# Kernel tuning notes

Measured on AMD Instinct MI355X. Metric: run time of the kernel, lower is better.

## Reference

```python
import jax, jax.numpy as jnp
import numpy as np

ALPHA = 0.2          # LeakyReLU negative slope
NEG_INF = -9e15      # mask value used by the original pygat implementation


def gat_layer(x, adj, W, a_src, a_dst, concat):
    """Dense multi-head GAT layer (pygat-style GraphAttentionLayer).

    x: [N, F_in], adj: [N, N] bool, W: [K, F_in, H], a_src/a_dst: [K, H].
    Returns [N, K*H] (concat=True, with ELU) or [N, H] (concat=False, mean heads).
    """
    h = jnp.einsum('nf,kfh->knh', x, W)                      # [K, N, H]
    f_src = jnp.einsum('knh,kh->kn', h, a_src)               # [K, N]
    f_dst = jnp.einsum('knh,kh->kn', h, a_dst)               # [K, N]
    e = jax.nn.leaky_relu(f_src[:, :, None] + f_dst[:, None, :], ALPHA)  # [K, N, N]
    e = jnp.where(adj[None, :, :], e, NEG_INF)
    att = jax.nn.softmax(e, axis=-1)                         # masked softmax over neighbors
    out = jnp.einsum('knm,kmh->knh', att, h)                 # [K, N, H]
    if concat:
        K, N, H = out.shape
        return jax.nn.elu(jnp.transpose(out, (1, 0, 2)).reshape(N, K * H))
    return out.mean(axis=0)                                  # [N, H]


def setup_inputs() -> dict:
    key = jax.random.key(0)
    ks = jax.random.split(key, 8)
    N, Fdim, H, K, C = 8192, 512, 128, 2, 16
    x = jax.random.normal(ks[0], (N, Fdim), dtype=jnp.float32)
    # sparse-ish binary adjacency, avg degree ~32, with self loops
    adj = jax.random.uniform(ks[1], (N, N)) < (32.0 / N)
    adj = adj | jnp.eye(N, dtype=bool)
    s1 = 1.0 / np.sqrt(Fdim)
    s2 = 1.0 / np.sqrt(K * H)
    W1 = jax.random.normal(ks[2], (K, Fdim, H), dtype=jnp.float32) * s1
    a1_src = jax.random.normal(ks[3], (K, H), dtype=jnp.float32) * s1
    a1_dst = jax.random.normal(ks[4], (K, H), dtype=jnp.float32) * s1
    W2 = jax.random.normal(ks[5], (1, K * H, C), dtype=jnp.float32) * s2
    a2_src = jax.random.normal(ks[6], (1, C), dtype=jnp.float32) * s2
    a2_dst = jax.random.normal(ks[7], (1, C), dtype=jnp.float32) * s2
    return {"x": x, "adj": adj, "W1": W1, "a1_src": a1_src, "a1_dst": a1_dst,
            "W2": W2, "a2_src": a2_src, "a2_dst": a2_dst}


def reference(x, adj, W1, a1_src, a1_dst, W2, a2_src, a2_dst):
    h1 = gat_layer(x, adj, W1, a1_src, a1_dst, concat=True)   # [N, K*H]
    h1 = jax.nn.relu(h1)                                      # dropout p=0.0 -> identity
    out = gat_layer(h1, adj, W2, a2_src, a2_dst, concat=False)  # [N, C]
    return out
```

## Files before the change

### kernel.cpp

```cpp
#include <hip/hip_runtime.h>
#include <hip/hip_bf16.h>
#include <math.h>

constexpr int NN   = 8192;
constexpr int FIN  = 512;
constexpr int HC   = 256;
constexpr int COUT = 16;
constexpr int MAXD = 128;

typedef __attribute__((ext_vector_type(8))) short bf16x8;
typedef __attribute__((ext_vector_type(4))) float f32x4;

__device__ __forceinline__ float lrelu(float x) { return x > 0.f ? x : 0.2f * x; }

__device__ __forceinline__ unsigned short f2bf(float f) {
  unsigned u = __float_as_uint(f);
  return (unsigned short)((u + 0x7fffu + ((u >> 16) & 1u)) >> 16);
}
__device__ __forceinline__ float bf2f(unsigned short h) {
  unsigned u = ((unsigned)h) << 16;
  return __uint_as_float(u);
}

__global__ __launch_bounds__(64) void detect_kernel(const int* __restrict__ adj32,
                                                    int* __restrict__ flag) {
  int lane = threadIdx.x;
  size_t idx = (size_t)(lane * 32) * (size_t)(NN + 1);
  int v = adj32[idx];
  bool four = (v == 1) || (v == 0x3f800000);
  unsigned long long b = __ballot(four);
  if (lane == 0) flag[0] = (b == ~0ull) ? 1 : 0;
}

__global__ __launch_bounds__(256) void build_csr(const void* __restrict__ adj,
                                                 const int* __restrict__ flag,
                                                 int* __restrict__ nbr,
                                                 int* __restrict__ cnt) {
  __shared__ int scnt;
  int i = blockIdx.x;
  if (threadIdx.x == 0) scnt = 0;
  __syncthreads();
  int* row_out = nbr + (size_t)i * MAXD;
  if (flag[0]) {
    const int4* row = reinterpret_cast<const int4*>((const int*)adj + (size_t)i * NN);
#pragma unroll
    for (int rep = 0; rep < 8; ++rep) {
      int vi = rep * 256 + threadIdx.x;
      int4 v = row[vi];
      int base = vi * 4;
      if (v.x) { int p = atomicAdd(&scnt, 1); if (p < MAXD) row_out[p] = base; }
      if (v.y) { int p = atomicAdd(&scnt, 1); if (p < MAXD) row_out[p] = base + 1; }
      if (v.z) { int p = atomicAdd(&scnt, 1); if (p < MAXD) row_out[p] = base + 2; }
      if (v.w) { int p = atomicAdd(&scnt, 1); if (p < MAXD) row_out[p] = base + 3; }
    }
  } else {
    const uint4* row = reinterpret_cast<const uint4*>((const unsigned char*)adj + (size_t)i * NN);
#pragma unroll
    for (int rep = 0; rep < 2; ++rep) {
      int vi = rep * 256 + threadIdx.x;
      uint4 v = row[vi];
      int base = vi * 16;
      unsigned w[4] = {v.x, v.y, v.z, v.w};
#pragma unroll
      for (int q = 0; q < 4; ++q)
#pragma unroll
        for (int b = 0; b < 4; ++b)
          if ((w[q] >> (8 * b)) & 0xffu) {
            int p = atomicAdd(&scnt, 1);
            if (p < MAXD) row_out[p] = base + q * 4 + b;
          }
    }
  }
  __syncthreads();
  if (threadIdx.x == 0) cnt[i] = scnt < MAXD ? scnt : MAXD;
}

__global__ __launch_bounds__(256) void convert_x(const float* __restrict__ x,
                                                 unsigned short* __restrict__ Xh,
                                                 unsigned short* __restrict__ Xl) {
  int t = blockIdx.x * 256 + threadIdx.x;
  float4 v = *reinterpret_cast<const float4*>(x + (size_t)t * 4);
  ushort4 hi, lo;
  hi.x = f2bf(v.x); lo.x = f2bf(v.x - bf2f(hi.x));
  hi.y = f2bf(v.y); lo.y = f2bf(v.y - bf2f(hi.y));
  hi.z = f2bf(v.z); lo.z = f2bf(v.z - bf2f(hi.z));
  hi.w = f2bf(v.w); lo.w = f2bf(v.w - bf2f(hi.w));
  *reinterpret_cast<ushort4*>(Xh + (size_t)t * 4) = hi;
  *reinterpret_cast<ushort4*>(Xl + (size_t)t * 4) = lo;
}

__global__ __launch_bounds__(256) void convert_w(const float* __restrict__ W1,
                                                 unsigned short* __restrict__ Wth,
                                                 unsigned short* __restrict__ Wtl) {
  int idx = blockIdx.x * 256 + threadIdx.x;
  int n = idx >> 9, kk = idx & 511;
  int k = n >> 7, h = n & 127;
  float v = W1[k * 65536 + kk * 128 + h];
  unsigned short hi = f2bf(v);
  Wth[idx] = hi;
  Wtl[idx] = f2bf(v - bf2f(hi));
}

__global__ __launch_bounds__(256) void gemm1m(const unsigned short* __restrict__ Xh,
                                              const unsigned short* __restrict__ Xl,
                                              const unsigned short* __restrict__ Bh,
                                              const unsigned short* __restrict__ Bl,
                                              float* __restrict__ Hout) {
  int wave = threadIdx.x >> 6, lane = threadIdx.x & 63;
  int rowBase = blockIdx.x * 128 + wave * 32;
  int colBase = blockIdx.y * 64;
  int frow = lane & 15;
  int kchunk = (lane >> 4) * 8;
  f32x4 acc[2][4] = {};
  for (int k0 = 0; k0 < FIN; k0 += 32) {
    bf16x8 ah[2], al[2], bh[4], bl[4];
#pragma unroll
    for (int r = 0; r < 2; ++r) {
      size_t off = (size_t)(rowBase + r * 16 + frow) * FIN + k0 + kchunk;
      ah[r] = *reinterpret_cast<const bf16x8*>(Xh + off);
      al[r] = *reinterpret_cast<const bf16x8*>(Xl + off);
    }
#pragma unroll
    for (int c = 0; c < 4; ++c) {
      size_t off = (size_t)(colBase + c * 16 + frow) * FIN + k0 + kchunk;
      bh[c] = *reinterpret_cast<const bf16x8*>(Bh + off);
      bl[c] = *reinterpret_cast<const bf16x8*>(Bl + off);
    }
#pragma unroll
    for (int r = 0; r < 2; ++r)
#pragma unroll
      for (int c = 0; c < 4; ++c) {
        acc[r][c] = __builtin_amdgcn_mfma_f32_16x16x32_bf16(ah[r], bh[c], acc[r][c], 0, 0, 0);
        acc[r][c] = __builtin_amdgcn_mfma_f32_16x16x32_bf16(ah[r], bl[c], acc[r][c], 0, 0, 0);
        acc[r][c] = __builtin_amdgcn_mfma_f32_16x16x32_bf16(al[r], bh[c], acc[r][c], 0, 0, 0);
      }
  }
  int dcol = lane & 15, drow4 = (lane >> 4) * 4;
#pragma unroll
  for (int r = 0; r < 2; ++r)
#pragma unroll
    for (int c = 0; c < 4; ++c)
#pragma unroll
      for (int q = 0; q < 4; ++q)
        Hout[(size_t)(rowBase + r * 16 + drow4 + q) * HC + colBase + c * 16 + dcol] =
            acc[r][c][q];
}

__global__ __launch_bounds__(256) void f1_kernel(const float* __restrict__ H,
                                                 const float* __restrict__ a_src,
                                                 const float* __restrict__ a_dst,
                                                 float* __restrict__ fs,
                                                 float* __restrict__ fd) {
  int wave = threadIdx.x >> 6, lane = threadIdx.x & 63;
  int n = blockIdx.x * 4 + wave;
  const float* hr = H + (size_t)n * HC;
  float h0 = hr[lane], h1 = hr[lane + 64], h2 = hr[lane + 128], h3 = hr[lane + 192];
  float s0 = h0 * a_src[lane] + h1 * a_src[lane + 64];
  float s1 = h2 * a_src[lane + 128] + h3 * a_src[lane + 192];
  float d0 = h0 * a_dst[lane] + h1 * a_dst[lane + 64];
  float d1 = h2 * a_dst[lane + 128] + h3 * a_dst[lane + 192];
#pragma unroll
  for (int off = 32; off > 0; off >>= 1) {
    s0 += __shfl_xor(s0, off);
    s1 += __shfl_xor(s1, off);
    d0 += __shfl_xor(d0, off);
    d1 += __shfl_xor(d1, off);
  }
  if (lane == 0) {
    fs[n] = s0; fs[NN + n] = s1;
    fd[n] = d0; fd[NN + n] = d1;
  }
}

__global__ __launch_bounds__(256) void attn1_kernel(const int* __restrict__ nbr,
                                                    const int* __restrict__ cnt,
                                                    const float* __restrict__ H,
                                                    const float* __restrict__ fs,
                                                    const float* __restrict__ fd,
                                                    float* __restrict__ H1) {
  __shared__ float att[2][MAXD];
  __shared__ int jidx[MAXD];
  int i = blockIdx.x;
  int t = threadIdx.x;
  int deg = cnt[i];
  if (t < MAXD && t < deg) {
    int j = nbr[(size_t)i * MAXD + t];
    jidx[t] = j;
    att[0][t] = lrelu(fs[i] + fd[j]);
    att[1][t] = lrelu(fs[NN + i] + fd[NN + j]);
  }
  __syncthreads();
  int wave = t >> 6, lane = t & 63;
  if (wave < 2) {
    int k = wave;
    float e0 = (lane < deg) ? att[k][lane] : -INFINITY;
    float e1 = (lane + 64 < deg) ? att[k][lane + 64] : -INFINITY;
    float m = fmaxf(e0, e1);
#pragma unroll
    for (int off = 32; off > 0; off >>= 1) m = fmaxf(m, __shfl_xor(m, off));
    float p0 = (lane < deg) ? expf(e0 - m) : 0.f;
    float p1 = (lane + 64 < deg) ? expf(e1 - m) : 0.f;
    float s = p0 + p1;
#pragma unroll
    for (int off = 32; off > 0; off >>= 1) s += __shfl_xor(s, off);
    float inv = 1.f / s;
    if (lane < deg) att[k][lane] = p0 * inv;
    if (lane + 64 < deg) att[k][lane + 64] = p1 * inv;
  }
  __syncthreads();
  int k = t >> 7;
  float acc = 0.f;
  int q = 0;
  for (; q + 4 <= deg; q += 4) {
    float a0 = att[k][q], a1 = att[k][q + 1], a2 = att[k][q + 2], a3 = att[k][q + 3];
    int j0 = jidx[q], j1 = jidx[q + 1], j2 = jidx[q + 2], j3 = jidx[q + 3];
    float g0 = H[(size_t)j0 * HC + t];
    float g1 = H[(size_t)j1 * HC + t];
    float g2 = H[(size_t)j2 * HC + t];
    float g3 = H[(size_t)j3 * HC + t];
    acc += a0 * g0 + a1 * g1 + a2 * g2 + a3 * g3;
  }
  for (; q < deg; ++q) acc += att[k][q] * H[(size_t)jidx[q] * HC + t];
  H1[(size_t)i * HC + t] = fmaxf(acc, 0.f);
}

__global__ __launch_bounds__(256) void gemm2_kernel(const float* __restrict__ H1,
                                                    const float* __restrict__ W2,
                                                    const float* __restrict__ a2s,
                                                    const float* __restrict__ a2d,
                                                    float* __restrict__ H2,
                                                    float* __restrict__ f2s,
                                                    float* __restrict__ f2d) {
  __shared__ float Ws[HC * COUT];
  int tid = threadIdx.x;
#pragma unroll
  for (int r = 0; r < 16; ++r) Ws[r * 256 + tid] = W2[r * 256 + tid];
  __syncthreads();
  int rg = tid >> 4, c = tid & 15;
  int n = blockIdx.x * 16 + rg;
  const float* h1r = H1 + (size_t)n * HC;
  float acc = 0.f;
#pragma unroll 8
  for (int kk = 0; kk < HC; ++kk) acc += h1r[kk] * Ws[kk * COUT + c];
  H2[(size_t)n * COUT + c] = acc;
  float s = acc * a2s[c];
  float d = acc * a2d[c];
#pragma unroll
  for (int off = 8; off > 0; off >>= 1) {
    s += __shfl_xor(s, off, 16);
    d += __shfl_xor(d, off, 16);
  }
  if (c == 0) { f2s[n] = s; f2d[n] = d; }
}

__global__ __launch_bounds__(64) void attn2_kernel(const int* __restrict__ nbr,
                                                   const int* __restrict__ cnt,
                                                   const float* __restrict__ H2,
                                                   const float* __restrict__ fs,
                                                   const float* __restrict__ fd,
                                                   float* __restrict__ out) {
  __shared__ float att[MAXD];
  __shared__ int jj[MAXD];
  int i = blockIdx.x;
  int lane = threadIdx.x;
  int deg = cnt[i];
  float fsi = fs[i];
  int j0 = (lane < deg) ? nbr[(size_t)i * MAXD + lane] : 0;
  int j1 = (lane + 64 < deg) ? nbr[(size_t)i * MAXD + lane + 64] : 0;
  float e0 = (lane < deg) ? lrelu(fsi + fd[j0]) : -INFINITY;
  float e1 = (lane + 64 < deg) ? lrelu(fsi + fd[j1]) : -INFINITY;
  float m = fmaxf(e0, e1);
#pragma unroll
  for (int off = 32; off > 0; off >>= 1) m = fmaxf(m, __shfl_xor(m, off));
  float p0 = (lane < deg) ? expf(e0 - m) : 0.f;
  float p1 = (lane + 64 < deg) ? expf(e1 - m) : 0.f;
  float s = p0 + p1;
#pragma unroll
  for (int off = 32; off > 0; off >>= 1) s += __shfl_xor(s, off);
  float inv = 1.f / s;
  att[lane] = p0 * inv;
  att[lane + 64] = p1 * inv;
  jj[lane] = j0;
  jj[lane + 64] = j1;
  __syncthreads();
  if (lane < COUT) {
    float acc = 0.f;
    for (int q = 0; q < deg; ++q) acc += att[q] * H2[(size_t)jj[q] * COUT + lane];
    out[(size_t)i * COUT + lane] = acc;
  }
}

extern "C" void kernel_launch(void* const* d_in, const int* in_sizes, int n_in,
                              void* d_out, int out_size, void* d_ws, size_t ws_size,
                              hipStream_t stream) {
  const float* x   = (const float*)d_in[0];
  const void*  adj = d_in[1];
  const float* W1  = (const float*)d_in[2];
  const float* a1s = (const float*)d_in[3];
  const float* a1d = (const float*)d_in[4];
  const float* W2  = (const float*)d_in[5];
  const float* a2s = (const float*)d_in[6];
  const float* a2d = (const float*)d_in[7];
  float* out = (float*)d_out;

  char* ws = (char*)d_ws;
  size_t off = 0;
  auto alloc = [&](size_t bytes) -> void* {
    void* p = ws + off;
    off = (off + bytes + 255) & ~(size_t)255;
    return p;
  };
  int*            flag = (int*)           alloc(4);
  int*            nbr  = (int*)           alloc((size_t)NN * MAXD * 4);
  int*            cnt  = (int*)           alloc((size_t)NN * 4);
  unsigned short* Xh   = (unsigned short*)alloc((size_t)NN * FIN * 2);
  unsigned short* Xl   = (unsigned short*)alloc((size_t)NN * FIN * 2);
  unsigned short* Wth  = (unsigned short*)alloc((size_t)HC * FIN * 2);
  unsigned short* Wtl  = (unsigned short*)alloc((size_t)HC * FIN * 2);
  float*          H    = (float*)         alloc((size_t)NN * HC * 4);
  float*          fs   = (float*)         alloc((size_t)2 * NN * 4);
  float*          fd   = (float*)         alloc((size_t)2 * NN * 4);
  float*          H1   = (float*)         alloc((size_t)NN * HC * 4);
  float*          H2   = (float*)         alloc((size_t)NN * COUT * 4);
  float*          f2s  = (float*)         alloc((size_t)NN * 4);
  float*          f2d  = (float*)         alloc((size_t)NN * 4);

  hipLaunchKernelGGL(detect_kernel, dim3(1), dim3(64), 0, stream, (const int*)adj, flag);
  hipLaunchKernelGGL(build_csr, dim3(NN), dim3(256), 0, stream, adj, flag, nbr, cnt);
  hipLaunchKernelGGL(convert_x, dim3(NN * FIN / 1024), dim3(256), 0, stream, x, Xh, Xl);
  hipLaunchKernelGGL(convert_w, dim3(HC * FIN / 256), dim3(256), 0, stream, W1, Wth, Wtl);
  hipLaunchKernelGGL(gemm1m, dim3(NN / 128, HC / 64), dim3(256), 0, stream, Xh, Xl, Wth, Wtl, H);
  hipLaunchKernelGGL(f1_kernel, dim3(NN / 4), dim3(256), 0, stream, H, a1s, a1d, fs, fd);
  hipLaunchKernelGGL(attn1_kernel, dim3(NN), dim3(256), 0, stream, nbr, cnt, H, fs, fd, H1);
  hipLaunchKernelGGL(gemm2_kernel, dim3(NN / 16), dim3(256), 0, stream, H1, W2, a2s, a2d, H2, f2s, f2d);
  hipLaunchKernelGGL(attn2_kernel, dim3(NN), dim3(64), 0, stream, nbr, cnt, H2, f2s, f2d, out);
}
```

Before: 459.4 us.

## Fuse prep kernels, inline dtype detection, fold attention logits into GEMM epilogue

Merges the x/W bf16 split conversions and the zeroing of fs/fd into one prep kernel. Moves adjacency dtype detection into each build_csr block, replacing the separate detect kernel and its global flag. Computes the per-node source/destination attention logits in the gemm1 epilogue with shuffles and atomicAdd, removing the f1 kernel's reread of H. This cuts three launches and one pass over H, at the cost of atomics and a redundant detection read in every CSR block.

```diff
diff --git a/kernel.cpp b/kernel.cpp
--- a/kernel.cpp
+++ b/kernel.cpp
@@ -22,30 +22,62 @@
   return __uint_as_float(u);
 }
 
-__global__ __launch_bounds__(64) void detect_kernel(const int* __restrict__ adj32,
-                                                    int* __restrict__ flag) {
-  int lane = threadIdx.x;
-  size_t idx = (size_t)(lane * 32) * (size_t)(NN + 1);
-  int v = adj32[idx];
-  bool four = (v == 1) || (v == 0x3f800000);
-  unsigned long long b = __ballot(four);
-  if (lane == 0) flag[0] = (b == ~0ull) ? 1 : 0;
+__global__ __launch_bounds__(256) void prep_kernel(const float* __restrict__ x,
+                                                   const float* __restrict__ W1,
+                                                   unsigned short* __restrict__ Xh,
+                                                   unsigned short* __restrict__ Xl,
+                                                   unsigned short* __restrict__ Wth,
+                                                   unsigned short* __restrict__ Wtl,
+                                                   float* __restrict__ fs,
+                                                   float* __restrict__ fd) {
+  int b = blockIdx.x;
+  if (b < 4096) {
+    int t = b * 256 + threadIdx.x;
+    float4 v = *reinterpret_cast<const float4*>(x + (size_t)t * 4);
+    ushort4 hi, lo;
+    hi.x = f2bf(v.x); lo.x = f2bf(v.x - bf2f(hi.x));
+    hi.y = f2bf(v.y); lo.y = f2bf(v.y - bf2f(hi.y));
+    hi.z = f2bf(v.z); lo.z = f2bf(v.z - bf2f(hi.z));
+    hi.w = f2bf(v.w); lo.w = f2bf(v.w - bf2f(hi.w));
+    *reinterpret_cast<ushort4*>(Xh + (size_t)t * 4) = hi;
+    *reinterpret_cast<ushort4*>(Xl + (size_t)t * 4) = lo;
+  } else if (b < 4608) {
+    int idx = (b - 4096) * 256 + threadIdx.x;
+    int n = idx >> 9, kk = idx & 511;
+    int k = n >> 7, h = n & 127;
+    float v = W1[k * 65536 + kk * 128 + h];
+    unsigned short hi = f2bf(v);
+    Wth[idx] = hi;
+    Wtl[idx] = f2bf(v - bf2f(hi));
+  } else {
+    int z = (b - 4608) * 256 + threadIdx.x;
+    if (z < 2 * NN) fs[z] = 0.f;
+    else fd[z - 2 * NN] = 0.f;
+  }
 }
 
 __global__ __launch_bounds__(256) void build_csr(const void* __restrict__ adj,
-                                                 const int* __restrict__ flag,
                                                  int* __restrict__ nbr,
                                                  int* __restrict__ cnt) {
   __shared__ int scnt;
+  __shared__ int sflag;
   int i = blockIdx.x;
-  if (threadIdx.x == 0) scnt = 0;
+  int t = threadIdx.x;
+  if (t == 0) scnt = 0;
+  if (t < 64) {
+    size_t idx = (size_t)(t * 32) * (size_t)(NN + 1);
+    int v = ((const int*)adj)[idx];
+    bool four = (v == 1) || (v == 0x3f800000);
+    unsigned long long b = __ballot(four);
+    if (t == 0) sflag = (b == ~0ull) ? 1 : 0;
+  }
   __syncthreads();
   int* row_out = nbr + (size_t)i * MAXD;
-  if (flag[0]) {
+  if (sflag) {
     const int4* row = reinterpret_cast<const int4*>((const int*)adj + (size_t)i * NN);
 #pragma unroll
     for (int rep = 0; rep < 8; ++rep) {
-      int vi = rep * 256 + threadIdx.x;
+      int vi = rep * 256 + t;
       int4 v = row[vi];
       int base = vi * 4;
       if (v.x) { int p = atomicAdd(&scnt, 1); if (p < MAXD) row_out[p] = base; }
@@ -57,55 +89,33 @@
     const uint4* row = reinterpret_cast<const uint4*>((const unsigned char*)adj + (size_t)i * NN);
 #pragma unroll
     for (int rep = 0; rep < 2; ++rep) {
-      int vi = rep * 256 + threadIdx.x;
+      int vi = rep * 256 + t;
       uint4 v = row[vi];
       int base = vi * 16;
       unsigned w[4] = {v.x, v.y, v.z, v.w};
 #pragma unroll
       for (int q = 0; q < 4; ++q)
 #pragma unroll
-        for (int b = 0; b < 4; ++b)
-          if ((w[q] >> (8 * b)) & 0xffu) {
+        for (int bb = 0; bb < 4; ++bb)
+          if ((w[q] >> (8 * bb)) & 0xffu) {
             int p = atomicAdd(&scnt, 1);
-            if (p < MAXD) row_out[p] = base + q * 4 + b;
+            if (p < MAXD) row_out[p] = base + q * 4 + bb;
           }
     }
   }
   __syncthreads();
-  if (threadIdx.x == 0) cnt[i] = scnt < MAXD ? scnt : MAXD;
-}
-
-__global__ __launch_bounds__(256) void convert_x(const float* __restrict__ x,
-                                                 unsigned short* __restrict__ Xh,
-                                                 unsigned short* __restrict__ Xl) {
-  int t = blockIdx.x * 256 + threadIdx.x;
-  float4 v = *reinterpret_cast<const float4*>(x + (size_t)t * 4);
-  ushort4 hi, lo;
-  hi.x = f2bf(v.x); lo.x = f2bf(v.x - bf2f(hi.x));
-  hi.y = f2bf(v.y); lo.y = f2bf(v.y - bf2f(hi.y));
-  hi.z = f2bf(v.z); lo.z = f2bf(v.z - bf2f(hi.z));
-  hi.w = f2bf(v.w); lo.w = f2bf(v.w - bf2f(hi.w));
-  *reinterpret_cast<ushort4*>(Xh + (size_t)t * 4) = hi;
-  *reinterpret_cast<ushort4*>(Xl + (size_t)t * 4) = lo;
-}
-
-__global__ __launch_bounds__(256) void convert_w(const float* __restrict__ W1,
-                                                 unsigned short* __restrict__ Wth,
-                                                 unsigned short* __restrict__ Wtl) {
-  int idx = blockIdx.x * 256 + threadIdx.x;
-  int n = idx >> 9, kk = idx & 511;
-  int k = n >> 7, h = n & 127;
-  float v = W1[k * 65536 + kk * 128 + h];
-  unsigned short hi = f2bf(v);
-  Wth[idx] = hi;
-  Wtl[idx] = f2bf(v - bf2f(hi));
+  if (t == 0) cnt[i] = scnt < MAXD ? scnt : MAXD;
 }
 
 __global__ __launch_bounds__(256) void gemm1m(const unsigned short* __restrict__ Xh,
                                               const unsigned short* __restrict__ Xl,
                                               const unsigned short* __restrict__ Bh,
                                               const unsigned short* __restrict__ Bl,
-                                              float* __restrict__ Hout) {
+                                              const float* __restrict__ a1s,
+                                              const float* __restrict__ a1d,
+                                              float* __restrict__ Hout,
+                                              float* __restrict__ fs,
+                                              float* __restrict__ fd) {
   int wave = threadIdx.x >> 6, lane = threadIdx.x & 63;
   int rowBase = blockIdx.x * 128 + wave * 32;
   int colBase = blockIdx.y * 64;
@@ -144,32 +154,35 @@
       for (int q = 0; q < 4; ++q)
         Hout[(size_t)(rowBase + r * 16 + drow4 + q) * HC + colBase + c * 16 + dcol] =
             acc[r][c][q];
-}
-
-__global__ __launch_bounds__(256) void f1_kernel(const float* __restrict__ H,
-                                                 const float* __restrict__ a_src,
-                                                 const float* __restrict__ a_dst,
-                                                 float* __restrict__ fs,
-                                                 float* __restrict__ fd) {
-  int wave = threadIdx.x >> 6, lane = threadIdx.x & 63;
-  int n = blockIdx.x * 4 + wave;
-  const float* hr = H + (size_t)n * HC;
-  float h0 = hr[lane], h1 = hr[lane + 64], h2 = hr[lane + 128], h3 = hr[lane + 192];
-  float s0 = h0 * a_src[lane] + h1 * a_src[lane + 64];
-  float s1 = h2 * a_src[lane + 128] + h3 * a_src[lane + 192];
-  float d0 = h0 * a_dst[lane] + h1 * a_dst[lane + 64];
-  float d1 = h2 * a_dst[lane + 128] + h3 * a_dst[lane + 192];
-#pragma unroll
-  for (int off = 32; off > 0; off >>= 1) {
-    s0 += __shfl_xor(s0, off);
-    s1 += __shfl_xor(s1, off);
-    d0 += __shfl_xor(d0, off);
-    d1 += __shfl_xor(d1, off);
-  }
-  if (lane == 0) {
-    fs[n] = s0; fs[NN + n] = s1;
-    fd[n] = d0; fd[NN + n] = d1;
-  }
+  int khead = colBase >> 7;
+  float as[4], ad[4];
+#pragma unroll
+  for (int c = 0; c < 4; ++c) {
+    as[c] = a1s[colBase + c * 16 + dcol];
+    ad[c] = a1d[colBase + c * 16 + dcol];
+  }
+#pragma unroll
+  for (int r = 0; r < 2; ++r)
+#pragma unroll
+    for (int q = 0; q < 4; ++q) {
+      float s = 0.f, d = 0.f;
+#pragma unroll
+      for (int c = 0; c < 4; ++c) {
+        float v = acc[r][c][q];
+        s += v * as[c];
+        d += v * ad[c];
+      }
+#pragma unroll
+      for (int off = 8; off > 0; off >>= 1) {
+        s += __shfl_xor(s, off, 16);
+        d += __shfl_xor(d, off, 16);
+      }
+      if ((lane & 15) == 0) {
+        int row = rowBase + r * 16 + drow4 + q;
+        atomicAdd(fs + khead * NN + row, s);
+        atomicAdd(fd + khead * NN + row, d);
+      }
+    }
 }
 
 __global__ __launch_bounds__(256) void attn1_kernel(const int* __restrict__ nbr,
@@ -310,7 +323,6 @@
     off = (off + bytes + 255) & ~(size_t)255;
     return p;
   };
-  int*            flag = (int*)           alloc(4);
   int*            nbr  = (int*)           alloc((size_t)NN * MAXD * 4);
   int*            cnt  = (int*)           alloc((size_t)NN * 4);
   unsigned short* Xh   = (unsigned short*)alloc((size_t)NN * FIN * 2);
@@ -325,12 +337,11 @@
   float*          f2s  = (float*)         alloc((size_t)NN * 4);
   float*          f2d  = (float*)         alloc((size_t)NN * 4);
 
-  hipLaunchKernelGGL(detect_kernel, dim3(1), dim3(64), 0, stream, (const int*)adj, flag);
-  hipLaunchKernelGGL(build_csr, dim3(NN), dim3(256), 0, stream, adj, flag, nbr, cnt);
-  hipLaunchKernelGGL(convert_x, dim3(NN * FIN / 1024), dim3(256), 0, stream, x, Xh, Xl);
-  hipLaunchKernelGGL(convert_w, dim3(HC * FIN / 256), dim3(256), 0, stream, W1, Wth, Wtl);
-  hipLaunchKernelGGL(gemm1m, dim3(NN / 128, HC / 64), dim3(256), 0, stream, Xh, Xl, Wth, Wtl, H);
-  hipLaunchKernelGGL(f1_kernel, dim3(NN / 4), dim3(256), 0, stream, H, a1s, a1d, fs, fd);
+  hipLaunchKernelGGL(prep_kernel, dim3(4736), dim3(256), 0, stream,
+                     x, W1, Xh, Xl, Wth, Wtl, fs, fd);
+  hipLaunchKernelGGL(build_csr, dim3(NN), dim3(256), 0, stream, adj, nbr, cnt);
+  hipLaunchKernelGGL(gemm1m, dim3(NN / 128, HC / 64), dim3(256), 0, stream,
+                     Xh, Xl, Wth, Wtl, a1s, a1d, H, fs, fd);
   hipLaunchKernelGGL(attn1_kernel, dim3(NN), dim3(256), 0, stream, nbr, cnt, H, fs, fd, H1);
   hipLaunchKernelGGL(gemm2_kernel, dim3(NN / 16), dim3(256), 0, stream, H1, W2, a2s, a2d, H2, f2s, f2d);
   hipLaunchKernelGGL(attn2_kernel, dim3(NN), dim3(64), 0, stream, nbr, cnt, H2, f2s, f2d, out);
```

New measurement: 456.8 us. No clear change (-0.6%).
